# Kernel optimization log

Measured on AMD Instinct MI355X. Metric: run time of the kernel, lower is better.

## Reference

```python
import jax, jax.numpy as jnp
import numpy as np

E = 12000          # edge_num
D = 49 * 128       # sphere_basis_reduce * sphere_channels_reduce
H = 256            # hidden_channel
C = 128            # sphere_channels_reduce


def setup_inputs() -> dict:
    key = jax.random.key(0)
    ks = jax.random.split(key, 7)
    scale1 = 1.0 / np.sqrt(D)
    scale2 = 1.0 / np.sqrt(H)
    return {
        "node_embed": jax.random.normal(ks[0], (E, D), jnp.float32),
        "x_edge_c": jax.random.normal(ks[1], (E, H), jnp.float32),
        "ori": jax.random.normal(ks[2], (E, D), jnp.float32),
        "W1": jax.random.normal(ks[3], (D, H), jnp.float32) * scale1,
        "b1": jax.random.normal(ks[4], (H,), jnp.float32) * scale1,
        "W2": jax.random.normal(ks[5], (H, D), jnp.float32) * scale2,
        "b2": jax.random.normal(ks[6], (D,), jnp.float32) * scale2,
        "edge_num": E,
    }


def reference(node_embed, x_edge_c, ori, W1, b1, W2, b2, edge_num):
    # cat along edge axis: [2E, D]
    x = jnp.concatenate([node_embed, ori], axis=0)
    # fc1 + SiLU: [2E, H]
    h = jax.nn.silu(x @ W1 + b1)
    # edge-gated multiply, x_edge_c broadcast across the 2-way cat axis
    h = (h.reshape(2, edge_num, H) * x_edge_c.reshape(1, edge_num, H)).reshape(-1, H)
    # fc2 + SiLU: [2E, D]
    y = jax.nn.silu(h @ W2 + b2)
    # split-and-add combine: [E, D/C, C]
    y = y.reshape(2 * edge_num, -1, C)
    return y[:edge_num] + y[edge_num:]
```

## Files before the change

kernel.cpp:

```cpp
#include <hip/hip_runtime.h>

#define E_NUM 12000
#define D_DIM 6272
#define H_DIM 256
#define M1 24000

typedef __attribute__((ext_vector_type(8))) short short8;
typedef __attribute__((ext_vector_type(8))) __bf16 bf16x8;
typedef __attribute__((ext_vector_type(4))) float f32x4;

__device__ __forceinline__ float silu_f(float x) {
  return x / (1.0f + __expf(-x));
}

__device__ __forceinline__ bf16x8 ld_frag(const short* p) {
  return __builtin_bit_cast(bf16x8, *(const short8*)p);
}

__device__ __forceinline__ bf16x8 cvt8(f32x4 a, f32x4 b) {
  bf16x8 r;
#pragma unroll
  for (int j = 0; j < 4; ++j) {
    r[j] = (__bf16)a[j];
    r[4 + j] = (__bf16)b[j];
  }
  return r;
}

__device__ __forceinline__ void gll16(const void* g, void* l) {
  __builtin_amdgcn_global_load_lds(
      (const __attribute__((address_space(1))) void*)g,
      (__attribute__((address_space(3))) void*)l, 16, 0, 0);
}

__global__ void pack_p1(const float* __restrict__ W1, short* __restrict__ P1) {
  const int kt = blockIdx.x;
  const int col = threadIdx.x;
  const float* src = W1 + (size_t)kt * 32 * H_DIM + col;
  short* dst = P1 + ((size_t)kt * H_DIM + col) * 32;
#pragma unroll
  for (int c = 0; c < 4; ++c) {
    short8 s;
#pragma unroll
    for (int j = 0; j < 8; ++j)
      s[j] = __builtin_bit_cast(short, (__bf16)src[(size_t)(c * 8 + j) * H_DIM]);
    *(short8*)(dst + c * 8) = s;
  }
}

__global__ void pack_p2(const float* __restrict__ W2, short* __restrict__ P2) {
  const int kt = blockIdx.y;
  const int col = blockIdx.x * 128 + threadIdx.x;
  const float* src = W2 + (size_t)kt * 32 * D_DIM + col;
  short* dst = P2 + ((size_t)kt * D_DIM + col) * 32;
#pragma unroll
  for (int c = 0; c < 4; ++c) {
    short8 s;
#pragma unroll
    for (int j = 0; j < 8; ++j)
      s[j] = __builtin_bit_cast(short, (__bf16)src[(size_t)(c * 8 + j) * D_DIM]);
    *(short8*)(dst + c * 8) = s;
  }
}

#define G1_NT 49
__launch_bounds__(256, 3)
__global__ void gemm1_kernel(const float* __restrict__ node_embed,
                             const float* __restrict__ ori,
                             const float* __restrict__ x_edge_c,
                             const short* __restrict__ P1,
                             const float* __restrict__ b1,
                             short* __restrict__ hgp) {
  __shared__ __align__(16) float Abuf[2][32 * 128];

  const int t = threadIdx.x;
  const int wn = t >> 6;
  const int lane = t & 63;
  const int l15 = lane & 15;
  const int lq = lane >> 4;
  const int m_base = blockIdx.x * 32;

  const float* xb = (m_base < E_NUM) ? (node_embed + (size_t)m_base * D_DIM)
                                     : (ori + (size_t)(m_base - E_NUM) * D_DIM);

  const float* aP =
      xb + (size_t)(t >> 5) * D_DIM + (((t & 24) | ((t & 7) ^ (t >> 5))) * 4);

  const short* bbase = P1 + (size_t)(wn * 64 + l15) * 32 + lq * 8;

  const int asw = l15 & 7;

  f32x4 acc[2][4];
#pragma unroll
  for (int m = 0; m < 2; ++m)
#pragma unroll
    for (int n = 0; n < 4; ++n) acc[m][n] = (f32x4){0.f, 0.f, 0.f, 0.f};

#define G1_STAGE(IT, BUF)                                                     \
  do {                                                                        \
    const float* _a = aP + (size_t)(IT)*128;                                  \
    gll16(_a, &Abuf[BUF][t * 4]);                                             \
    gll16(_a + (size_t)8 * D_DIM, &Abuf[BUF][t * 4 + 1024]);                  \
    gll16(_a + (size_t)16 * D_DIM, &Abuf[BUF][t * 4 + 2048]);                 \
    gll16(_a + (size_t)24 * D_DIM, &Abuf[BUF][t * 4 + 3072]);                 \
  } while (0)

  G1_STAGE(0, 0);
  __syncthreads();

  int cur = 0;
  for (int it = 0; it < G1_NT; ++it) {
    const int nxt = cur ^ 1;

    bf16x8 bq[4][4];
    {
      const short* bs = bbase + (size_t)it * 32768;
#pragma unroll
      for (int ks = 0; ks < 4; ++ks)
#pragma unroll
        for (int n = 0; n < 4; ++n) bq[ks][n] = ld_frag(bs + ks * 8192 + n * 512);
    }

    if (it + 1 < G1_NT) G1_STAGE(it + 1, nxt);

    const float* Ap = &Abuf[cur][0];
#pragma unroll
    for (int ks = 0; ks < 4; ++ks) {
      bf16x8 af[2];
#pragma unroll
      for (int m = 0; m < 2; ++m) {
        const int row = m * 16 + l15;
        const int c_lo = 8 * ks + 2 * lq;
        const int pl = (c_lo & 24) | ((c_lo & 7) ^ asw);
        const int ph = (c_lo & 24) | (((c_lo + 1) & 7) ^ asw);
        f32x4 lo = *(const f32x4*)(Ap + row * 128 + pl * 4);
        f32x4 hi = *(const f32x4*)(Ap + row * 128 + ph * 4);
        af[m] = cvt8(lo, hi);
      }
#pragma unroll
      for (int m = 0; m < 2; ++m)
#pragma unroll
        for (int n = 0; n < 4; ++n)
          acc[m][n] = __builtin_amdgcn_mfma_f32_16x16x32_bf16(af[m], bq[ks][n],
                                                              acc[m][n], 0, 0, 0);
    }
    __syncthreads();
    cur = nxt;
  }

#pragma unroll
  for (int n = 0; n < 4; ++n) {
    const int col = wn * 64 + n * 16 + l15;
    const float b1v = b1[col];
    const int panel = wn * 2 + (n >> 1);
    const int cin = (n & 1) * 16 + l15;
#pragma unroll
    for (int m = 0; m < 2; ++m) {
#pragma unroll
      for (int i = 0; i < 4; ++i) {
        const int gmr = m_base + m * 16 + lq * 4 + i;
        const int e = (gmr < E_NUM) ? gmr : gmr - E_NUM;
        float v = acc[m][n][i] + b1v;
        v = silu_f(v) * x_edge_c[(size_t)e * H_DIM + col];
        hgp[((size_t)panel * M1 + gmr) * 32 + cin] = __builtin_bit_cast(short, (__bf16)v);
      }
    }
  }
#undef G1_STAGE
}

__launch_bounds__(256, 2)
__global__ void gemm2_kernel(const short* __restrict__ hgp,
                             const short* __restrict__ P2,
                             const float* __restrict__ b2,
                             float* __restrict__ out) {
  __shared__ __align__(16) short Ah[128 * 256];

  const int t = threadIdx.x;
  const int wd = t >> 6;
  const int lane = t & 63;
  const int l15 = lane & 15;
  const int lq = lane >> 4;
  const int d0 = blockIdx.x * 128;
  const int e0 = blockIdx.y * 64;

  const int lc = (t & 24) | ((t & 7) ^ (t >> 5));
#pragma unroll
  for (int j = 0; j < 16; ++j) {
    const int arow = j * 8 + (t >> 5);
    int e = e0 + (arow & 63);
    if (e >= E_NUM) e = E_NUM - 1;
    const int grow = (arow < 64) ? e : (E_NUM + e);
    const short* src = hgp + ((size_t)(lc >> 2) * M1 + grow) * 32 + (lc & 3) * 8;
    gll16(src, &Ah[(j * 256 + t) * 8]);
  }
  __syncthreads();

  f32x4 acc[8][2];
#pragma unroll
  for (int m = 0; m < 8; ++m)
#pragma unroll
    for (int n = 0; n < 2; ++n) acc[m][n] = (f32x4){0.f, 0.f, 0.f, 0.f};

  const int asw = l15 & 7;
#pragma unroll
  for (int kk = 0; kk < 8; ++kk) {
    bf16x8 bq[2];
#pragma unroll
    for (int n = 0; n < 2; ++n)
      bq[n] = ld_frag(P2 + (size_t)kk * ((size_t)D_DIM * 32) +
                      (size_t)(d0 + wd * 32 + n * 16 + l15) * 32 + lq * 8);
#pragma unroll
    for (int m = 0; m < 8; ++m) {
      const int row = (m & 3) * 16 + (m >> 2) * 64 + l15;
      const int c = kk * 4 + lq;
      const int pc = (c & 24) | ((c & 7) ^ asw);
      bf16x8 af = ld_frag(&Ah[row * 256 + pc * 8]);
      acc[m][0] = __builtin_amdgcn_mfma_f32_16x16x32_bf16(af, bq[0], acc[m][0], 0, 0, 0);
      acc[m][1] = __builtin_amdgcn_mfma_f32_16x16x32_bf16(af, bq[1], acc[m][1], 0, 0, 0);
    }
  }

#pragma unroll
  for (int n = 0; n < 2; ++n) {
    const int col = d0 + wd * 32 + n * 16 + l15;
    const float b2v = b2[col];
#pragma unroll
    for (int mm = 0; mm < 4; ++mm) {
#pragma unroll
      for (int i = 0; i < 4; ++i) {
        const int e = e0 + mm * 16 + lq * 4 + i;
        if (e < E_NUM) {
          out[(size_t)e * D_DIM + col] =
              silu_f(acc[mm][n][i] + b2v) + silu_f(acc[mm + 4][n][i] + b2v);
        }
      }
    }
  }
}

extern "C" void kernel_launch(void* const* d_in, const int* in_sizes, int n_in,
                              void* d_out, int out_size, void* d_ws, size_t ws_size,
                              hipStream_t stream) {
  const float* node_embed = (const float*)d_in[0];
  const float* x_edge_c = (const float*)d_in[1];
  const float* ori = (const float*)d_in[2];
  const float* W1 = (const float*)d_in[3];
  const float* b1 = (const float*)d_in[4];
  const float* W2 = (const float*)d_in[5];
  const float* b2 = (const float*)d_in[6];
  float* out_p = (float*)d_out;

  char* ws = (char*)d_ws;
  short* P1 = (short*)ws;
  short* P2 = (short*)(ws + 3211264);
  short* hgp = (short*)(ws + 2 * 3211264);

  pack_p1<<<dim3(D_DIM / 32), 256, 0, stream>>>(W1, P1);
  pack_p2<<<dim3(D_DIM / 128, 8), 128, 0, stream>>>(W2, P2);

  gemm1_kernel<<<dim3(M1 / 32), 256, 0, stream>>>(node_embed, ori, x_edge_c, P1, b1, hgp);

  gemm2_kernel<<<dim3(D_DIM / 128, (E_NUM + 63) / 64), 256, 0, stream>>>(hgp, P2, b2, out_p);
}
```

Before: 466.7 us.

## Fuse fc1 and fc2 GEMMs into one kernel keeping hidden tile in LDS

Merges the two GEMM kernels into one. Each block handles 16 edges, pairing node_embed and ori rows, and stores the gated hidden tile in swizzled LDS instead of writing it to global memory. Each wave then computes a quarter of the fc2 output columns straight from LDS and does the split-add. This removes the hidden-activation round trip and one launch. The cost is that every block re-reads all of W2 (P2), which greatly raises L2 traffic, and fc2 tiles become small (32 rows), so MFMA reuse per weight load drops.

```diff
diff --git a/kernel.cpp b/kernel.cpp
--- a/kernel.cpp
+++ b/kernel.cpp
@@ -65,29 +65,29 @@
 
 #define G1_NT 49
 __launch_bounds__(256, 3)
-__global__ void gemm1_kernel(const float* __restrict__ node_embed,
+__global__ void fused_kernel(const float* __restrict__ node_embed,
+                             const float* __restrict__ x_edge_c,
                              const float* __restrict__ ori,
-                             const float* __restrict__ x_edge_c,
                              const short* __restrict__ P1,
                              const float* __restrict__ b1,
-                             short* __restrict__ hgp) {
+                             const short* __restrict__ P2,
+                             const float* __restrict__ b2,
+                             float* __restrict__ out) {
   __shared__ __align__(16) float Abuf[2][32 * 128];
+  __shared__ __align__(16) short hls[32 * 256];
 
   const int t = threadIdx.x;
   const int wn = t >> 6;
   const int lane = t & 63;
   const int l15 = lane & 15;
   const int lq = lane >> 4;
-  const int m_base = blockIdx.x * 32;
-
-  const float* xb = (m_base < E_NUM) ? (node_embed + (size_t)m_base * D_DIM)
-                                     : (ori + (size_t)(m_base - E_NUM) * D_DIM);
-
-  const float* aP =
-      xb + (size_t)(t >> 5) * D_DIM + (((t & 24) | ((t & 7) ^ (t >> 5))) * 4);
+  const int e0 = blockIdx.x * 16;
+
+  const int aswz_chunk = ((t & 24) | ((t & 7) ^ (t >> 5)));
+  const float* aNE = node_embed + (size_t)(e0 + (t >> 5)) * D_DIM + aswz_chunk * 4;
+  const float* aOR = ori + (size_t)(e0 + (t >> 5)) * D_DIM + aswz_chunk * 4;
 
   const short* bbase = P1 + (size_t)(wn * 64 + l15) * 32 + lq * 8;
-
   const int asw = l15 & 7;
 
   f32x4 acc[2][4];
@@ -96,13 +96,14 @@
 #pragma unroll
     for (int n = 0; n < 4; ++n) acc[m][n] = (f32x4){0.f, 0.f, 0.f, 0.f};
 
-#define G1_STAGE(IT, BUF)                                                     \
-  do {                                                                        \
-    const float* _a = aP + (size_t)(IT)*128;                                  \
-    gll16(_a, &Abuf[BUF][t * 4]);                                             \
-    gll16(_a + (size_t)8 * D_DIM, &Abuf[BUF][t * 4 + 1024]);                  \
-    gll16(_a + (size_t)16 * D_DIM, &Abuf[BUF][t * 4 + 2048]);                 \
-    gll16(_a + (size_t)24 * D_DIM, &Abuf[BUF][t * 4 + 3072]);                 \
+#define G1_STAGE(IT, BUF)                                                 \
+  do {                                                                    \
+    const float* _n = aNE + (size_t)(IT)*128;                             \
+    const float* _o = aOR + (size_t)(IT)*128;                             \
+    gll16(_n, &Abuf[BUF][t * 4]);                                         \
+    gll16(_n + (size_t)8 * D_DIM, &Abuf[BUF][t * 4 + 1024]);              \
+    gll16(_o, &Abuf[BUF][t * 4 + 2048]);                                  \
+    gll16(_o + (size_t)8 * D_DIM, &Abuf[BUF][t * 4 + 3072]);              \
   } while (0)
 
   G1_STAGE(0, 0);
@@ -111,7 +112,6 @@
   int cur = 0;
   for (int it = 0; it < G1_NT; ++it) {
     const int nxt = cur ^ 1;
-
     bf16x8 bq[4][4];
     {
       const short* bs = bbase + (size_t)it * 32768;
@@ -120,7 +120,6 @@
 #pragma unroll
         for (int n = 0; n < 4; ++n) bq[ks][n] = ld_frag(bs + ks * 8192 + n * 512);
     }
-
     if (it + 1 < G1_NT) G1_STAGE(it + 1, nxt);
 
     const float* Ap = &Abuf[cur][0];
@@ -147,93 +146,66 @@
     __syncthreads();
     cur = nxt;
   }
+#undef G1_STAGE
 
 #pragma unroll
   for (int n = 0; n < 4; ++n) {
     const int col = wn * 64 + n * 16 + l15;
     const float b1v = b1[col];
-    const int panel = wn * 2 + (n >> 1);
-    const int cin = (n & 1) * 16 + l15;
+    const int hc = col >> 3;
 #pragma unroll
     for (int m = 0; m < 2; ++m) {
 #pragma unroll
       for (int i = 0; i < 4; ++i) {
-        const int gmr = m_base + m * 16 + lq * 4 + i;
-        const int e = (gmr < E_NUM) ? gmr : gmr - E_NUM;
+        const int row = m * 16 + lq * 4 + i;
+        const int e = e0 + (row & 15);
         float v = acc[m][n][i] + b1v;
         v = silu_f(v) * x_edge_c[(size_t)e * H_DIM + col];
-        hgp[((size_t)panel * M1 + gmr) * 32 + cin] = __builtin_bit_cast(short, (__bf16)v);
+        const int pc = (hc & 16) | ((hc & 15) ^ (row & 15));
+        hls[row * 256 + pc * 8 + (col & 7)] = __builtin_bit_cast(short, (__bf16)v);
       }
     }
   }
-#undef G1_STAGE
-}
-
-__launch_bounds__(256, 2)
-__global__ void gemm2_kernel(const short* __restrict__ hgp,
-                             const short* __restrict__ P2,
-                             const float* __restrict__ b2,
-                             float* __restrict__ out) {
-  __shared__ __align__(16) short Ah[128 * 256];
-
-  const int t = threadIdx.x;
-  const int wd = t >> 6;
-  const int lane = t & 63;
-  const int l15 = lane & 15;
-  const int lq = lane >> 4;
-  const int d0 = blockIdx.x * 128;
-  const int e0 = blockIdx.y * 64;
-
-  const int lc = (t & 24) | ((t & 7) ^ (t >> 5));
-#pragma unroll
-  for (int j = 0; j < 16; ++j) {
-    const int arow = j * 8 + (t >> 5);
-    int e = e0 + (arow & 63);
-    if (e >= E_NUM) e = E_NUM - 1;
-    const int grow = (arow < 64) ? e : (E_NUM + e);
-    const short* src = hgp + ((size_t)(lc >> 2) * M1 + grow) * 32 + (lc & 3) * 8;
-    gll16(src, &Ah[(j * 256 + t) * 8]);
-  }
   __syncthreads();
 
-  f32x4 acc[8][2];
-#pragma unroll
-  for (int m = 0; m < 8; ++m)
-#pragma unroll
-    for (int n = 0; n < 2; ++n) acc[m][n] = (f32x4){0.f, 0.f, 0.f, 0.f};
-
-  const int asw = l15 & 7;
-#pragma unroll
-  for (int kk = 0; kk < 8; ++kk) {
-    bf16x8 bq[2];
-#pragma unroll
-    for (int n = 0; n < 2; ++n)
-      bq[n] = ld_frag(P2 + (size_t)kk * ((size_t)D_DIM * 32) +
-                      (size_t)(d0 + wd * 32 + n * 16 + l15) * 32 + lq * 8);
-#pragma unroll
-    for (int m = 0; m < 8; ++m) {
-      const int row = (m & 3) * 16 + (m >> 2) * 64 + l15;
-      const int c = kk * 4 + lq;
-      const int pc = (c & 24) | ((c & 7) ^ asw);
-      bf16x8 af = ld_frag(&Ah[row * 256 + pc * 8]);
-      acc[m][0] = __builtin_amdgcn_mfma_f32_16x16x32_bf16(af, bq[0], acc[m][0], 0, 0, 0);
-      acc[m][1] = __builtin_amdgcn_mfma_f32_16x16x32_bf16(af, bq[1], acc[m][1], 0, 0, 0);
-    }
-  }
-
-#pragma unroll
-  for (int n = 0; n < 2; ++n) {
-    const int col = d0 + wd * 32 + n * 16 + l15;
-    const float b2v = b2[col];
-#pragma unroll
-    for (int mm = 0; mm < 4; ++mm) {
+  const int dstart = wn * 1568;
+  for (int c = 0; c < 49; ++c) {
+    const int dbase = dstart + c * 32;
+    bf16x8 bq2[8][2];
+#pragma unroll
+    for (int kk = 0; kk < 8; ++kk)
+#pragma unroll
+      for (int n = 0; n < 2; ++n)
+        bq2[kk][n] =
+            ld_frag(P2 + ((size_t)kk * D_DIM + dbase + n * 16 + l15) * 32 + lq * 8);
+
+    f32x4 a2[2][2];
+#pragma unroll
+    for (int m = 0; m < 2; ++m)
+#pragma unroll
+      for (int n = 0; n < 2; ++n) a2[m][n] = (f32x4){0.f, 0.f, 0.f, 0.f};
+
+#pragma unroll
+    for (int kk = 0; kk < 8; ++kk) {
+      const int c2 = kk * 4 + lq;
+      const int p2 = (c2 & 16) | ((c2 & 15) ^ l15);
+      bf16x8 af0 = ld_frag(&hls[(0 * 16 + l15) * 256 + p2 * 8]);
+      bf16x8 af1 = ld_frag(&hls[(1 * 16 + l15) * 256 + p2 * 8]);
+      a2[0][0] = __builtin_amdgcn_mfma_f32_16x16x32_bf16(af0, bq2[kk][0], a2[0][0], 0, 0, 0);
+      a2[0][1] = __builtin_amdgcn_mfma_f32_16x16x32_bf16(af0, bq2[kk][1], a2[0][1], 0, 0, 0);
+      a2[1][0] = __builtin_amdgcn_mfma_f32_16x16x32_bf16(af1, bq2[kk][0], a2[1][0], 0, 0, 0);
+      a2[1][1] = __builtin_amdgcn_mfma_f32_16x16x32_bf16(af1, bq2[kk][1], a2[1][1], 0, 0, 0);
+    }
+
+#pragma unroll
+    for (int n = 0; n < 2; ++n) {
+      const int col = dbase + n * 16 + l15;
+      const float b2v = b2[col];
 #pragma unroll
       for (int i = 0; i < 4; ++i) {
-        const int e = e0 + mm * 16 + lq * 4 + i;
-        if (e < E_NUM) {
-          out[(size_t)e * D_DIM + col] =
-              silu_f(acc[mm][n][i] + b2v) + silu_f(acc[mm + 4][n][i] + b2v);
-        }
+        const int e = e0 + lq * 4 + i;
+        out[(size_t)e * D_DIM + col] =
+            silu_f(a2[0][n][i] + b2v) + silu_f(a2[1][n][i] + b2v);
       }
     }
   }
@@ -254,12 +226,10 @@
   char* ws = (char*)d_ws;
   short* P1 = (short*)ws;
   short* P2 = (short*)(ws + 3211264);
-  short* hgp = (short*)(ws + 2 * 3211264);
 
   pack_p1<<<dim3(D_DIM / 32), 256, 0, stream>>>(W1, P1);
   pack_p2<<<dim3(D_DIM / 128, 8), 128, 0, stream>>>(W2, P2);
 
-  gemm1_kernel<<<dim3(M1 / 32), 256, 0, stream>>>(node_embed, ori, x_edge_c, P1, b1, hgp);
-
-  gemm2_kernel<<<dim3(D_DIM / 128, (E_NUM + 63) / 64), 256, 0, stream>>>(hgp, P2, b2, out_p);
-}
+  fused_kernel<<<dim3(E_NUM / 16), 256, 0, stream>>>(node_embed, x_edge_c, ori, P1,
+                                                     b1, P2, b2, out_p);
+}
```

Measured after the change: 433.3 us. 7.2% less time.

## Triple-buffer LDS staging of A and B tiles in both GEMM kernels

Applied to the files above, without the earlier changes.

Both GEMM kernels move to a three-stage LDS ring fed by global_load_lds, with explicit vmcnt waits and raw barriers. In gemm1 the K tile drops from 128 to 32 and the packed W1 panels are now staged through swizzled LDS instead of being read straight into registers. In gemm2 the whole-K A preload is replaced by a pipelined K loop that also stages P2 tiles in LDS. The goal is to overlap global loads with MFMA work and cut register pressure. The cost is four times as many iterations and barriers in gemm1, and hand-tuned wait counts that must match the number of in-flight loads exactly.

```diff
diff --git a/kernel.cpp b/kernel.cpp
--- a/kernel.cpp
+++ b/kernel.cpp
@@ -63,15 +63,16 @@
   }
 }
 
-#define G1_NT 49
-__launch_bounds__(256, 3)
+#define G1_NT 196
+__launch_bounds__(256, 2)
 __global__ void gemm1_kernel(const float* __restrict__ node_embed,
                              const float* __restrict__ ori,
                              const float* __restrict__ x_edge_c,
                              const short* __restrict__ P1,
                              const float* __restrict__ b1,
                              short* __restrict__ hgp) {
-  __shared__ __align__(16) float Abuf[2][32 * 128];
+  __shared__ __align__(16) float Abuf[3][32 * 32];
+  __shared__ __align__(16) short Bbuf[3][256 * 32];
 
   const int t = threadIdx.x;
   const int wn = t >> 6;
@@ -80,15 +81,19 @@
   const int lq = lane >> 4;
   const int m_base = blockIdx.x * 32;
 
+  const int ar = t >> 3;
+  const int ag = (t & 7) ^ (ar & 7);
   const float* xb = (m_base < E_NUM) ? (node_embed + (size_t)m_base * D_DIM)
                                      : (ori + (size_t)(m_base - E_NUM) * D_DIM);
-
-  const float* aP =
-      xb + (size_t)(t >> 5) * D_DIM + (((t & 24) | ((t & 7) ^ (t >> 5))) * 4);
-
-  const short* bbase = P1 + (size_t)(wn * 64 + l15) * 32 + lq * 8;
-
-  const int asw = l15 & 7;
+  const float* asrc = xb + (size_t)ar * D_DIM + ag * 4;
+
+  const short* bsrc[4];
+#pragma unroll
+  for (int j = 0; j < 4; ++j) {
+    const int cl = (t >> 2) + j * 64;
+    const int g = (t & 3) ^ (cl & 3);
+    bsrc[j] = P1 + (size_t)cl * 32 + g * 8;
+  }
 
   f32x4 acc[2][4];
 #pragma unroll
@@ -96,57 +101,59 @@
 #pragma unroll
     for (int n = 0; n < 4; ++n) acc[m][n] = (f32x4){0.f, 0.f, 0.f, 0.f};
 
-#define G1_STAGE(IT, BUF)                                                     \
-  do {                                                                        \
-    const float* _a = aP + (size_t)(IT)*128;                                  \
-    gll16(_a, &Abuf[BUF][t * 4]);                                             \
-    gll16(_a + (size_t)8 * D_DIM, &Abuf[BUF][t * 4 + 1024]);                  \
-    gll16(_a + (size_t)16 * D_DIM, &Abuf[BUF][t * 4 + 2048]);                 \
-    gll16(_a + (size_t)24 * D_DIM, &Abuf[BUF][t * 4 + 3072]);                 \
+#define G1_STAGE(IT, BUF)                                                   \
+  do {                                                                      \
+    gll16(asrc + (size_t)(IT) * 32, &Abuf[BUF][t * 4]);                     \
+    const size_t _bo = (size_t)(IT) * 8192;                                 \
+    gll16(bsrc[0] + _bo, &Bbuf[BUF][t * 8]);                                \
+    gll16(bsrc[1] + _bo, &Bbuf[BUF][t * 8 + 2048]);                         \
+    gll16(bsrc[2] + _bo, &Bbuf[BUF][t * 8 + 4096]);                         \
+    gll16(bsrc[3] + _bo, &Bbuf[BUF][t * 8 + 6144]);                         \
   } while (0)
 
+#define G1_COMPUTE(BUF)                                                     \
+  do {                                                                      \
+    const float* Ap = &Abuf[BUF][0];                                        \
+    const short* Bp = &Bbuf[BUF][0];                                        \
+    bf16x8 af[2];                                                           \
+    _Pragma("unroll") for (int m = 0; m < 2; ++m) {                         \
+      const int r = m * 16 + l15;                                           \
+      f32x4 lo = *(const f32x4*)(Ap + r * 32 + (((2 * lq) ^ (l15 & 7)) * 4)); \
+      f32x4 hi = *(const f32x4*)(Ap + r * 32 + (((2 * lq + 1) ^ (l15 & 7)) * 4)); \
+      af[m] = cvt8(lo, hi);                                                 \
+    }                                                                       \
+    bf16x8 bq[4];                                                           \
+    _Pragma("unroll") for (int n = 0; n < 4; ++n) {                         \
+      const int col = wn * 64 + n * 16 + l15;                               \
+      bq[n] = ld_frag(Bp + col * 32 + ((lq ^ (col & 3)) * 8));              \
+    }                                                                       \
+    _Pragma("unroll") for (int m = 0; m < 2; ++m)                           \
+      _Pragma("unroll") for (int n = 0; n < 4; ++n)                         \
+        acc[m][n] = __builtin_amdgcn_mfma_f32_16x16x32_bf16(af[m], bq[n],   \
+                                                            acc[m][n], 0, 0, 0); \
+  } while (0)
+
   G1_STAGE(0, 0);
-  __syncthreads();
-
-  int cur = 0;
-  for (int it = 0; it < G1_NT; ++it) {
-    const int nxt = cur ^ 1;
-
-    bf16x8 bq[4][4];
-    {
-      const short* bs = bbase + (size_t)it * 32768;
-#pragma unroll
-      for (int ks = 0; ks < 4; ++ks)
-#pragma unroll
-        for (int n = 0; n < 4; ++n) bq[ks][n] = ld_frag(bs + ks * 8192 + n * 512);
+  G1_STAGE(1, 1);
+
+  int bsel = 0;
+  for (int it = 0; it < G1_NT - 1; ++it) {
+    asm volatile("s_waitcnt vmcnt(5)" ::: "memory");
+    __builtin_amdgcn_sched_barrier(0);
+    __builtin_amdgcn_s_barrier();
+    __builtin_amdgcn_sched_barrier(0);
+    G1_COMPUTE(bsel);
+    if (it + 2 < G1_NT) {
+      const int nb = (bsel + 2) % 3;
+      G1_STAGE(it + 2, nb);
     }
-
-    if (it + 1 < G1_NT) G1_STAGE(it + 1, nxt);
-
-    const float* Ap = &Abuf[cur][0];
-#pragma unroll
-    for (int ks = 0; ks < 4; ++ks) {
-      bf16x8 af[2];
-#pragma unroll
-      for (int m = 0; m < 2; ++m) {
-        const int row = m * 16 + l15;
-        const int c_lo = 8 * ks + 2 * lq;
-        const int pl = (c_lo & 24) | ((c_lo & 7) ^ asw);
-        const int ph = (c_lo & 24) | (((c_lo + 1) & 7) ^ asw);
-        f32x4 lo = *(const f32x4*)(Ap + row * 128 + pl * 4);
-        f32x4 hi = *(const f32x4*)(Ap + row * 128 + ph * 4);
-        af[m] = cvt8(lo, hi);
-      }
-#pragma unroll
-      for (int m = 0; m < 2; ++m)
-#pragma unroll
-        for (int n = 0; n < 4; ++n)
-          acc[m][n] = __builtin_amdgcn_mfma_f32_16x16x32_bf16(af[m], bq[ks][n],
-                                                              acc[m][n], 0, 0, 0);
-    }
-    __syncthreads();
-    cur = nxt;
-  }
+    bsel = (bsel == 2) ? 0 : bsel + 1;
+  }
+  asm volatile("s_waitcnt vmcnt(0)" ::: "memory");
+  __builtin_amdgcn_sched_barrier(0);
+  __builtin_amdgcn_s_barrier();
+  __builtin_amdgcn_sched_barrier(0);
+  G1_COMPUTE(bsel);
 
 #pragma unroll
   for (int n = 0; n < 4; ++n) {
@@ -167,14 +174,17 @@
     }
   }
 #undef G1_STAGE
-}
-
-__launch_bounds__(256, 2)
+#undef G1_COMPUTE
+}
+
+#define G2_NT 8
+__launch_bounds__(256, 3)
 __global__ void gemm2_kernel(const short* __restrict__ hgp,
                              const short* __restrict__ P2,
                              const float* __restrict__ b2,
                              float* __restrict__ out) {
-  __shared__ __align__(16) short Ah[128 * 256];
+  __shared__ __align__(16) short Abuf[3][128 * 32];
+  __shared__ __align__(16) short Bbuf[3][128 * 32];
 
   const int t = threadIdx.x;
   const int wd = t >> 6;
@@ -184,17 +194,19 @@
   const int d0 = blockIdx.x * 128;
   const int e0 = blockIdx.y * 64;
 
-  const int lc = (t & 24) | ((t & 7) ^ (t >> 5));
-#pragma unroll
-  for (int j = 0; j < 16; ++j) {
-    const int arow = j * 8 + (t >> 5);
-    int e = e0 + (arow & 63);
+  const int sr = t >> 2;
+  const short* asrc[2];
+  const short* bsrc[2];
+#pragma unroll
+  for (int j = 0; j < 2; ++j) {
+    const int row = sr + j * 64;
+    const int g = (t & 3) ^ (row & 3);
+    int e = e0 + sr;
     if (e >= E_NUM) e = E_NUM - 1;
-    const int grow = (arow < 64) ? e : (E_NUM + e);
-    const short* src = hgp + ((size_t)(lc >> 2) * M1 + grow) * 32 + (lc & 3) * 8;
-    gll16(src, &Ah[(j * 256 + t) * 8]);
-  }
-  __syncthreads();
+    const int grow = (j == 0) ? e : (E_NUM + e);
+    asrc[j] = hgp + (size_t)grow * 32 + g * 8;
+    bsrc[j] = P2 + (size_t)(d0 + row) * 32 + g * 8;
+  }
 
   f32x4 acc[8][2];
 #pragma unroll
@@ -202,24 +214,55 @@
 #pragma unroll
     for (int n = 0; n < 2; ++n) acc[m][n] = (f32x4){0.f, 0.f, 0.f, 0.f};
 
-  const int asw = l15 & 7;
-#pragma unroll
-  for (int kk = 0; kk < 8; ++kk) {
-    bf16x8 bq[2];
-#pragma unroll
-    for (int n = 0; n < 2; ++n)
-      bq[n] = ld_frag(P2 + (size_t)kk * ((size_t)D_DIM * 32) +
-                      (size_t)(d0 + wd * 32 + n * 16 + l15) * 32 + lq * 8);
-#pragma unroll
-    for (int m = 0; m < 8; ++m) {
-      const int row = (m & 3) * 16 + (m >> 2) * 64 + l15;
-      const int c = kk * 4 + lq;
-      const int pc = (c & 24) | ((c & 7) ^ asw);
-      bf16x8 af = ld_frag(&Ah[row * 256 + pc * 8]);
-      acc[m][0] = __builtin_amdgcn_mfma_f32_16x16x32_bf16(af, bq[0], acc[m][0], 0, 0, 0);
-      acc[m][1] = __builtin_amdgcn_mfma_f32_16x16x32_bf16(af, bq[1], acc[m][1], 0, 0, 0);
+#define G2_STAGE(IT, BUF)                                                   \
+  do {                                                                      \
+    const size_t _ka = (size_t)(IT) * (M1 * 32);                            \
+    const size_t _kb = (size_t)(IT) * ((size_t)D_DIM * 32);                 \
+    gll16(asrc[0] + _ka, &Abuf[BUF][t * 8]);                                \
+    gll16(asrc[1] + _ka, &Abuf[BUF][t * 8 + 2048]);                         \
+    gll16(bsrc[0] + _kb, &Bbuf[BUF][t * 8]);                                \
+    gll16(bsrc[1] + _kb, &Bbuf[BUF][t * 8 + 2048]);                         \
+  } while (0)
+
+#define G2_COMPUTE(BUF)                                                     \
+  do {                                                                      \
+    const short* Ap = &Abuf[BUF][0];                                        \
+    const short* Bp = &Bbuf[BUF][0];                                        \
+    bf16x8 bq[2];                                                           \
+    _Pragma("unroll") for (int n = 0; n < 2; ++n) {                         \
+      const int cl = wd * 32 + n * 16 + l15;                                \
+      bq[n] = ld_frag(Bp + cl * 32 + ((lq ^ (cl & 3)) * 8));                \
+    }                                                                       \
+    _Pragma("unroll") for (int m = 0; m < 8; ++m) {                         \
+      const int r = m * 16 + l15;                                           \
+      bf16x8 af = ld_frag(Ap + r * 32 + ((lq ^ (l15 & 3)) * 8));            \
+      _Pragma("unroll") for (int n = 0; n < 2; ++n)                         \
+        acc[m][n] = __builtin_amdgcn_mfma_f32_16x16x32_bf16(af, bq[n],      \
+                                                            acc[m][n], 0, 0, 0); \
+    }                                                                       \
+  } while (0)
+
+  G2_STAGE(0, 0);
+  G2_STAGE(1, 1);
+
+  int bsel = 0;
+  for (int it = 0; it < G2_NT - 1; ++it) {
+    asm volatile("s_waitcnt vmcnt(4)" ::: "memory");
+    __builtin_amdgcn_sched_barrier(0);
+    __builtin_amdgcn_s_barrier();
+    __builtin_amdgcn_sched_barrier(0);
+    G2_COMPUTE(bsel);
+    if (it + 2 < G2_NT) {
+      const int nb = (bsel + 2) % 3;
+      G2_STAGE(it + 2, nb);
     }
-  }
+    bsel = (bsel == 2) ? 0 : bsel + 1;
+  }
+  asm volatile("s_waitcnt vmcnt(0)" ::: "memory");
+  __builtin_amdgcn_sched_barrier(0);
+  __builtin_amdgcn_s_barrier();
+  __builtin_amdgcn_sched_barrier(0);
+  G2_COMPUTE(bsel);
 
 #pragma unroll
   for (int n = 0; n < 2; ++n) {
@@ -237,6 +280,8 @@
       }
     }
   }
+#undef G2_STAGE
+#undef G2_COMPUTE
 }
 
 extern "C" void kernel_launch(void* const* d_in, const int* in_sizes, int n_in,
```

After: 550.0 us. 1.18x slower.
